# Kernel tuning notes

Hardware: AMD Instinct MI355X
Metric: run time of the kernel (lower is better)

## Reference

```python
import jax, jax.numpy as jnp
import numpy as np

N_NODES = 50000
N_EDGES = 800000
IN_F, HID, OUT = 128, 128, 64


def setup_inputs() -> dict:
    key = jax.random.key(0)
    ks = jax.random.split(key, 12)
    sc = 0.05
    return {
        "features": jax.random.normal(ks[0], (N_NODES, IN_F), jnp.float32),
        "src": jax.random.randint(ks[1], (N_EDGES,), 0, N_NODES, jnp.int32),
        "dst": jax.random.randint(ks[2], (N_EDGES,), 0, N_NODES, jnp.int32),
        "Wself0": jax.random.normal(ks[3], (IN_F, HID), jnp.float32) * sc,
        "Wneigh0": jax.random.normal(ks[4], (IN_F, HID), jnp.float32) * sc,
        "b0": jnp.zeros((HID,), jnp.float32),
        "Wself1": jax.random.normal(ks[5], (HID, HID), jnp.float32) * sc,
        "Wneigh1": jax.random.normal(ks[6], (HID, HID), jnp.float32) * sc,
        "b1": jnp.zeros((HID,), jnp.float32),
        "Wself2": jax.random.normal(ks[7], (HID, OUT), jnp.float32) * sc,
        "Wneigh2": jax.random.normal(ks[8], (HID, OUT), jnp.float32) * sc,
        "b2": jnp.zeros((OUT,), jnp.float32),
    }


def _sage_conv(h, src, dst, Ws, Wn, b, act):
    # mean aggregator: mean over in-neighbors (src -> dst), zero for isolated nodes
    msg = h[src]                                            # [E, d] gather
    agg = jax.ops.segment_sum(msg, dst, num_segments=N_NODES)
    deg = jax.ops.segment_sum(jnp.ones((msg.shape[0],), h.dtype), dst,
                              num_segments=N_NODES)
    mean = agg / jnp.maximum(deg, 1.0)[:, None]             # [N, d]
    out = h @ Ws + mean @ Wn + b                            # fc_self + fc_neigh + bias
    return jax.nn.relu(out) if act else out


def reference(features, src, dst, Wself0, Wneigh0, b0, Wself1, Wneigh1, b1,
              Wself2, Wneigh2, b2):
    h = _sage_conv(features, src, dst, Wself0, Wneigh0, b0, True)
    h = _sage_conv(h, src, dst, Wself1, Wneigh1, b1, True)
    h = _sage_conv(h, src, dst, Wself2, Wneigh2, b2, False)
    return h
```

## Files before the change

### kernel.cpp

```cpp
#include <hip/hip_runtime.h>
#include <hip/hip_fp16.h>

#define N_NODES_C 50000
#define N_EDGES_C 800000
#define K_FEAT 128
#define HM_STRIDE 256
#define NB_C 196

typedef unsigned int uint_t;
typedef _Float16 half8 __attribute__((ext_vector_type(8)));
typedef _Float16 half4 __attribute__((ext_vector_type(4)));
typedef float f32x4 __attribute__((ext_vector_type(4)));


__global__ __launch_bounds__(256) void p1hist_conv_kernel(
    const int* __restrict__ dst, uint_t* __restrict__ histG, int E,
    const float* __restrict__ feat, _Float16* __restrict__ hm0,
    const float* __restrict__ Ws0, const float* __restrict__ Wn0,
    const float* __restrict__ Ws1, const float* __restrict__ Wn1,
    const float* __restrict__ Ws2, const float* __restrict__ Wn2,
    _Float16* __restrict__ WT0, _Float16* __restrict__ WT1, _Float16* __restrict__ WT2) {
    const int t = threadIdx.x, b = blockIdx.x;
    if (b < NB_C) {
        __shared__ uint_t hist[256];
        hist[t] = 0;
        __syncthreads();
        const int base = b * 4096;
#pragma unroll
        for (int j = 0; j < 16; ++j) {
            int idx = base + t + j * 256;
            if (idx < E) atomicAdd(&hist[((uint_t)dst[idx]) >> 8], 1u);
        }
        __syncthreads();
        histG[b * 256 + t] = hist[t];
    } else {
        const int i = (b - NB_C) * 256 + t;
        const int n4 = N_NODES_C * K_FEAT / 4;
        if (i < n4) {
            float4 v = reinterpret_cast<const float4*>(feat)[i];
            int n = i >> 5, c4 = i & 31;
            half4 o;
            o.x = (_Float16)v.x; o.y = (_Float16)v.y; o.z = (_Float16)v.z; o.w = (_Float16)v.w;
            *reinterpret_cast<half4*>(hm0 + (size_t)n * HM_STRIDE + c4 * 4) = o;
        } else {
            int idx = i - n4;
            if (idx >= 81920) return;
            const float* Ws;
            const float* Wn;
            _Float16* WT;
            int ncol;
            if (idx < 32768) { Ws = Ws0; Wn = Wn0; WT = WT0; ncol = 128; }
            else if (idx < 65536) { idx -= 32768; Ws = Ws1; Wn = Wn1; WT = WT1; ncol = 128; }
            else { idx -= 65536; Ws = Ws2; Wn = Wn2; WT = WT2; ncol = 64; }
            int k = idx & 255, c = idx >> 8;
            float v = (k < 128) ? Ws[(size_t)k * ncol + c] : Wn[(size_t)(k - 128) * ncol + c];
            WT[(size_t)c * 256 + k] = (_Float16)v;
        }
    }
}

__global__ __launch_bounds__(256) void p1scan_kernel(uint_t* __restrict__ histG,
                                                     uint_t* __restrict__ cbase) {
    const int t = threadIdx.x;
    uint_t run = 0;
    for (int bb = 0; bb < NB_C; bb += 28) {
        uint_t vals[28];
#pragma unroll
        for (int j = 0; j < 28; ++j) vals[j] = histG[(size_t)(bb + j) * 256 + t];
#pragma unroll
        for (int j = 0; j < 28; ++j) {
            uint_t x = vals[j];
            vals[j] = run;
            run += x;
        }
#pragma unroll
        for (int j = 0; j < 28; ++j) histG[(size_t)(bb + j) * 256 + t] = vals[j];
    }
    const int lane = t & 63, wid = t >> 6;
    uint_t x = run;
#pragma unroll
    for (int off = 1; off < 64; off <<= 1) {
        uint_t y = __shfl_up(x, off, 64);
        if (lane >= off) x += y;
    }
    __shared__ uint_t wsum[4];
    if (lane == 63) wsum[wid] = x;
    __syncthreads();
    uint_t wpre = 0;
#pragma unroll
    for (int w = 0; w < 4; ++w)
        if (w < wid) wpre += wsum[w];
    uint_t incl = wpre + x;
    cbase[t] = incl - run;
    if (t == 255) cbase[256] = incl;
}

__global__ __launch_bounds__(256) void p1scatter_kernel(const int* __restrict__ src,
                                                        const int* __restrict__ dst,
                                                        const uint_t* __restrict__ histG,
                                                        const uint_t* __restrict__ cbase,
                                                        uint_t* __restrict__ tmp, int E) {
    __shared__ uint_t cur[256];
    const int t = threadIdx.x, b = blockIdx.x;
    cur[t] = histG[b * 256 + t] + cbase[t];
    __syncthreads();
    const int base = b * 4096;
#pragma unroll
    for (int j = 0; j < 16; ++j) {
        int idx = base + t + j * 256;
        if (idx < E) {
            uint_t d = (uint_t)dst[idx];
            uint_t s = (uint_t)src[idx];
            uint_t slot = atomicAdd(&cur[d >> 8], 1u);
            tmp[slot] = ((d & 255u) << 16) | s;
        }
    }
}

__global__ __launch_bounds__(256) void p2_kernel(const uint_t* __restrict__ tmp,
                                                 const uint_t* __restrict__ cbase,
                                                 int* __restrict__ offs, int* __restrict__ ssrc) {
    __shared__ uint_t hist[256];
    __shared__ uint_t cur[256];
    __shared__ uint_t wsum[4];
    const int t = threadIdx.x, c = blockIdx.x;
    const uint_t cb = cbase[c], ce = cbase[c + 1];
    hist[t] = 0;
    __syncthreads();
    for (uint_t i = cb + t; i < ce; i += 256) atomicAdd(&hist[tmp[i] >> 16], 1u);
    __syncthreads();
    const uint_t v = hist[t];
    const int lane = t & 63, wid = t >> 6;
    uint_t x = v;
#pragma unroll
    for (int off = 1; off < 64; off <<= 1) {
        uint_t y = __shfl_up(x, off, 64);
        if (lane >= off) x += y;
    }
    if (lane == 63) wsum[wid] = x;
    __syncthreads();
    uint_t wpre = 0;
#pragma unroll
    for (int w = 0; w < 4; ++w)
        if (w < wid) wpre += wsum[w];
    const uint_t excl = wpre + x - v;
    const int node = c * 256 + t;
    if (node < N_NODES_C) offs[node] = (int)(cb + excl);
    if (c == 0 && t == 0) offs[N_NODES_C] = N_EDGES_C;
    cur[t] = excl;
    __syncthreads();
    for (uint_t i = cb + t; i < ce; i += 256) {
        uint_t p = tmp[i];
        uint_t slot = cb + atomicAdd(&cur[p >> 16], 1u);
        ssrc[slot] = (int)(p & 0xFFFFu);
    }
}


__global__ void mean_kernel(_Float16* __restrict__ hm, const int* __restrict__ offs,
                            const int* __restrict__ ssrc) {
    const int node = (int)((blockIdx.x * blockDim.x + threadIdx.x) >> 6);
    const int lane = threadIdx.x & 63;
    if (node >= N_NODES_C) return;
    const int beg = offs[node], end = offs[node + 1];
    const int g = lane >> 4;
    const int cb = (lane & 15) * 8;
    const _Float16* base = hm + cb;

    float accA[8] = {0.f, 0.f, 0.f, 0.f, 0.f, 0.f, 0.f, 0.f};
    float accB[8] = {0.f, 0.f, 0.f, 0.f, 0.f, 0.f, 0.f, 0.f};

    int e = beg;
    for (; e + 16 <= end; e += 16) {
        const int s0 = ssrc[e + g];
        const int s1 = ssrc[e + 4 + g];
        const int s2 = ssrc[e + 8 + g];
        const int s3 = ssrc[e + 12 + g];
        half8 v0 = *reinterpret_cast<const half8*>(base + (size_t)s0 * HM_STRIDE);
        half8 v1 = *reinterpret_cast<const half8*>(base + (size_t)s1 * HM_STRIDE);
        half8 v2 = *reinterpret_cast<const half8*>(base + (size_t)s2 * HM_STRIDE);
        half8 v3 = *reinterpret_cast<const half8*>(base + (size_t)s3 * HM_STRIDE);
#pragma unroll
        for (int j = 0; j < 8; ++j) accA[j] += (float)v0[j];
#pragma unroll
        for (int j = 0; j < 8; ++j) accB[j] += (float)v1[j];
#pragma unroll
        for (int j = 0; j < 8; ++j) accA[j] += (float)v2[j];
#pragma unroll
        for (int j = 0; j < 8; ++j) accB[j] += (float)v3[j];
    }
    for (; e + 8 <= end; e += 8) {
        const int s0 = ssrc[e + g];
        const int s1 = ssrc[e + 4 + g];
        half8 v0 = *reinterpret_cast<const half8*>(base + (size_t)s0 * HM_STRIDE);
        half8 v1 = *reinterpret_cast<const half8*>(base + (size_t)s1 * HM_STRIDE);
#pragma unroll
        for (int j = 0; j < 8; ++j) accA[j] += (float)v0[j];
#pragma unroll
        for (int j = 0; j < 8; ++j) accB[j] += (float)v1[j];
    }
    for (; e + 4 <= end; e += 4) {
        const int s0 = ssrc[e + g];
        half8 v0 = *reinterpret_cast<const half8*>(base + (size_t)s0 * HM_STRIDE);
#pragma unroll
        for (int j = 0; j < 8; ++j) accA[j] += (float)v0[j];
    }
    if (e < end) {
        const bool valid = (e + g) < end;
        const int s0 = valid ? ssrc[e + g] : ssrc[beg];
        half8 v0 = *reinterpret_cast<const half8*>(base + (size_t)s0 * HM_STRIDE);
        if (valid) {
#pragma unroll
            for (int j = 0; j < 8; ++j) accB[j] += (float)v0[j];
        }
    }

    const float inv = (end > beg) ? 1.0f / (float)(end - beg) : 0.f;
    half8 o;
#pragma unroll
    for (int j = 0; j < 8; ++j) {
        float x = accA[j] + accB[j];
        x += __shfl_xor(x, 16, 64);
        x += __shfl_xor(x, 32, 64);
        o[j] = (_Float16)(x * inv);
    }
    if (lane < 16)
        *reinterpret_cast<half8*>(hm + (size_t)node * HM_STRIDE + 128 + cb) = o;
}


template <int NCOL, bool ACT, bool OUT_FP32>
__global__ __launch_bounds__(256) void sage_mfma(
    const _Float16* __restrict__ hm,
    const _Float16* __restrict__ WT,
    const float* __restrict__ bias,
    float* __restrict__ outf,
    _Float16* __restrict__ outh,
    int nNodes) {
    constexpr int CF = NCOL / 16;
    constexpr int RPB = 128;

    __shared__ _Float16 bl[NCOL][256];

    const int t = threadIdx.x;
#pragma unroll
    for (int it = 0; it < NCOL * 32 / 256; ++it) {
        int f = t + it * 256;
        int row = f >> 5, c8 = f & 31;
        half8 v = *reinterpret_cast<const half8*>(WT + (size_t)row * 256 + c8 * 8);
        int col = (c8 * 8) ^ ((row & 7) << 3);
        *reinterpret_cast<half8*>(&bl[row][col]) = v;
    }
    __syncthreads();

    const int wid = t >> 6;
    const int lane = t & 63;
    const int r0 = blockIdx.x * RPB + wid * 32;
    const int koff = (lane >> 4) * 8;

    half8 a[2][8];
#pragma unroll
    for (int fr = 0; fr < 2; ++fr) {
        int row = r0 + fr * 16 + (lane & 15);
        if (row >= nNodes) row = nNodes - 1;
        const _Float16* ap = hm + (size_t)row * HM_STRIDE + koff;
#pragma unroll
        for (int ks = 0; ks < 8; ++ks)
            a[fr][ks] = *reinterpret_cast<const half8*>(ap + ks * 32);
    }

    f32x4 acc[2][CF];
#pragma unroll
    for (int fr = 0; fr < 2; ++fr)
#pragma unroll
        for (int c = 0; c < CF; ++c) acc[fr][c] = {0.f, 0.f, 0.f, 0.f};

#pragma unroll
    for (int c = 0; c < CF; ++c) {
        const int brow = c * 16 + (lane & 15);
        const int bswz = (brow & 7) << 3;
#pragma unroll
        for (int ks = 0; ks < 8; ++ks) {
            half8 b = *reinterpret_cast<const half8*>(&bl[brow][(ks * 32 + koff) ^ bswz]);
            acc[0][c] = __builtin_amdgcn_mfma_f32_16x16x32_f16(a[0][ks], b, acc[0][c], 0, 0, 0);
            acc[1][c] = __builtin_amdgcn_mfma_f32_16x16x32_f16(a[1][ks], b, acc[1][c], 0, 0, 0);
        }
    }

    const int ocol = lane & 15;
    const int orow_off = (lane >> 4) << 2;
#pragma unroll
    for (int fr = 0; fr < 2; ++fr) {
        const int rbase = r0 + fr * 16 + orow_off;
#pragma unroll
        for (int c = 0; c < CF; ++c) {
            const int col = c * 16 + ocol;
            const float bv = bias[col];
#pragma unroll
            for (int reg = 0; reg < 4; ++reg) {
                const int row = rbase + reg;
                if (row < nNodes) {
                    float v = acc[fr][c][reg] + bv;
                    if (ACT) v = fmaxf(v, 0.f);
                    if (OUT_FP32) outf[(size_t)row * NCOL + col] = v;
                    else outh[(size_t)row * HM_STRIDE + col] = (_Float16)v;
                }
            }
        }
    }
}


extern "C" void kernel_launch(void* const* d_in, const int* in_sizes, int n_in,
                              void* d_out, int out_size, void* d_ws, size_t ws_size,
                              hipStream_t stream) {
    const float* feat = (const float*)d_in[0];
    const int* src = (const int*)d_in[1];
    const int* dst = (const int*)d_in[2];
    const float* Ws0 = (const float*)d_in[3];
    const float* Wn0 = (const float*)d_in[4];
    const float* b0 = (const float*)d_in[5];
    const float* Ws1 = (const float*)d_in[6];
    const float* Wn1 = (const float*)d_in[7];
    const float* b1 = (const float*)d_in[8];
    const float* Ws2 = (const float*)d_in[9];
    const float* Wn2 = (const float*)d_in[10];
    const float* b2 = (const float*)d_in[11];
    float* out = (float*)d_out;

    auto align_up = [](size_t x) { return (x + 255) & ~(size_t)255; };
    char* w = (char*)d_ws;
    uint_t* histG = (uint_t*)w; w += align_up((size_t)NB_C * 256 * 4);
    uint_t* cbase = (uint_t*)w; w += align_up(257 * 4);
    uint_t* tmp = (uint_t*)w;   w += align_up((size_t)N_EDGES_C * 4);
    int* offs = (int*)w;        w += align_up((size_t)(N_NODES_C + 1) * 4);
    int* ssrc = (int*)w;        w += align_up((size_t)N_EDGES_C * 4);
    _Float16* hm0 = (_Float16*)w; w += align_up((size_t)N_NODES_C * HM_STRIDE * 2);
    _Float16* hm1 = (_Float16*)w; w += align_up((size_t)N_NODES_C * HM_STRIDE * 2);
    _Float16* WT0 = (_Float16*)w; w += align_up((size_t)128 * 256 * 2);
    _Float16* WT1 = (_Float16*)w; w += align_up((size_t)128 * 256 * 2);
    _Float16* WT2 = (_Float16*)w; w += align_up((size_t)64 * 256 * 2);
    _Float16* hm2 = hm0;

    const int convBlocks = (N_NODES_C * K_FEAT / 4 + 81920 + 255) / 256;
    p1hist_conv_kernel<<<NB_C + convBlocks, 256, 0, stream>>>(
        dst, histG, N_EDGES_C, feat, hm0, Ws0, Wn0, Ws1, Wn1, Ws2, Wn2, WT0, WT1, WT2);
    p1scan_kernel<<<1, 256, 0, stream>>>(histG, cbase);
    p1scatter_kernel<<<NB_C, 256, 0, stream>>>(src, dst, histG, cbase, tmp, N_EDGES_C);
    p2_kernel<<<NB_C, 256, 0, stream>>>(tmp, cbase, offs, ssrc);

    const int meanBlocks = (N_NODES_C * 64 + 255) / 256;
    const int gemmBlocks = (N_NODES_C + 127) / 128;

    mean_kernel<<<meanBlocks, 256, 0, stream>>>(hm0, offs, ssrc);
    sage_mfma<128, true, false><<<gemmBlocks, 256, 0, stream>>>(
        hm0, WT0, b0, nullptr, hm1, N_NODES_C);

    mean_kernel<<<meanBlocks, 256, 0, stream>>>(hm1, offs, ssrc);
    sage_mfma<128, true, false><<<gemmBlocks, 256, 0, stream>>>(
        hm1, WT1, b1, nullptr, hm2, N_NODES_C);

    mean_kernel<<<meanBlocks, 256, 0, stream>>>(hm2, offs, ssrc);
    sage_mfma<64, false, true><<<gemmBlocks, 256, 0, stream>>>(
        hm2, WT2, b2, out, nullptr, N_NODES_C);
}
```

Baseline: 167.6 us.

## Quantize node features to int8 with per-row scales for neighbor gather

Adds a per-node int8 copy of the features with one fp32 scale per row. It is produced in the conversion kernel and in each GEMM epilogue, and the mean aggregation now gathers these 8-byte int8 vectors plus a scale instead of 16-byte fp16 vectors. The aim is to halve the bytes moved by the random neighbor gather, which dominates the mean kernels. The cost is extra quantization stores and shuffles in the epilogues, an extra scale load per edge, and a loss of accuracy from 8-bit features that may exceed tolerance.

New measurement: 154.9 us. 7.6% less time.

```diff
diff --git a/kernel.cpp b/kernel.cpp
--- a/kernel.cpp
+++ b/kernel.cpp
@@ -8,6 +8,8 @@
 #define NB_C 196
 
 typedef unsigned int uint_t;
+typedef signed char schar;
+typedef schar schar8 __attribute__((ext_vector_type(8)));
 typedef _Float16 half8 __attribute__((ext_vector_type(8)));
 typedef _Float16 half4 __attribute__((ext_vector_type(4)));
 typedef float f32x4 __attribute__((ext_vector_type(4)));
@@ -16,6 +18,7 @@
 __global__ __launch_bounds__(256) void p1hist_conv_kernel(
     const int* __restrict__ dst, uint_t* __restrict__ histG, int E,
     const float* __restrict__ feat, _Float16* __restrict__ hm0,
+    schar* __restrict__ q0, float* __restrict__ sc0,
     const float* __restrict__ Ws0, const float* __restrict__ Wn0,
     const float* __restrict__ Ws1, const float* __restrict__ Wn1,
     const float* __restrict__ Ws2, const float* __restrict__ Wn2,
@@ -42,6 +45,19 @@
             half4 o;
             o.x = (_Float16)v.x; o.y = (_Float16)v.y; o.z = (_Float16)v.z; o.w = (_Float16)v.w;
             *reinterpret_cast<half4*>(hm0 + (size_t)n * HM_STRIDE + c4 * 4) = o;
+            float m = fmaxf(fmaxf(fabsf(v.x), fabsf(v.y)), fmaxf(fabsf(v.z), fabsf(v.w)));
+            m = fmaxf(m, __shfl_xor(m, 1, 64));
+            m = fmaxf(m, __shfl_xor(m, 2, 64));
+            m = fmaxf(m, __shfl_xor(m, 4, 64));
+            m = fmaxf(m, __shfl_xor(m, 8, 64));
+            m = fmaxf(m, __shfl_xor(m, 16, 64));
+            const float inv = (m > 0.f) ? 127.0f / m : 0.f;
+            uint_t w = ((uint_t)(unsigned char)(schar)rintf(v.x * inv)) |
+                       ((uint_t)(unsigned char)(schar)rintf(v.y * inv) << 8) |
+                       ((uint_t)(unsigned char)(schar)rintf(v.z * inv) << 16) |
+                       ((uint_t)(unsigned char)(schar)rintf(v.w * inv) << 24);
+            *reinterpret_cast<uint_t*>(q0 + (size_t)n * 128 + c4 * 4) = w;
+            if ((t & 31) == 0) sc0[n] = m * (1.0f / 127.0f);
         } else {
             int idx = i - n4;
             if (idx >= 81920) return;
@@ -157,7 +173,8 @@
 }
 
 
-__global__ void mean_kernel(_Float16* __restrict__ hm, const int* __restrict__ offs,
+__global__ void mean_kernel(const schar* __restrict__ q, const float* __restrict__ qsc,
+                            _Float16* __restrict__ hm, const int* __restrict__ offs,
                             const int* __restrict__ ssrc) {
     const int node = (int)((blockIdx.x * blockDim.x + threadIdx.x) >> 6);
     const int lane = threadIdx.x & 63;
@@ -165,7 +182,7 @@
     const int beg = offs[node], end = offs[node + 1];
     const int g = lane >> 4;
     const int cb = (lane & 15) * 8;
-    const _Float16* base = hm + cb;
+    const schar* base = q + cb;
 
     float accA[8] = {0.f, 0.f, 0.f, 0.f, 0.f, 0.f, 0.f, 0.f};
     float accB[8] = {0.f, 0.f, 0.f, 0.f, 0.f, 0.f, 0.f, 0.f};
@@ -176,43 +193,45 @@
         const int s1 = ssrc[e + 4 + g];
         const int s2 = ssrc[e + 8 + g];
         const int s3 = ssrc[e + 12 + g];
-        half8 v0 = *reinterpret_cast<const half8*>(base + (size_t)s0 * HM_STRIDE);
-        half8 v1 = *reinterpret_cast<const half8*>(base + (size_t)s1 * HM_STRIDE);
-        half8 v2 = *reinterpret_cast<const half8*>(base + (size_t)s2 * HM_STRIDE);
-        half8 v3 = *reinterpret_cast<const half8*>(base + (size_t)s3 * HM_STRIDE);
-#pragma unroll
-        for (int j = 0; j < 8; ++j) accA[j] += (float)v0[j];
-#pragma unroll
-        for (int j = 0; j < 8; ++j) accB[j] += (float)v1[j];
-#pragma unroll
-        for (int j = 0; j < 8; ++j) accA[j] += (float)v2[j];
-#pragma unroll
-        for (int j = 0; j < 8; ++j) accB[j] += (float)v3[j];
+        const float c0 = qsc[s0], c1 = qsc[s1], c2 = qsc[s2], c3 = qsc[s3];
+        schar8 v0 = *reinterpret_cast<const schar8*>(base + (size_t)s0 * 128);
+        schar8 v1 = *reinterpret_cast<const schar8*>(base + (size_t)s1 * 128);
+        schar8 v2 = *reinterpret_cast<const schar8*>(base + (size_t)s2 * 128);
+        schar8 v3 = *reinterpret_cast<const schar8*>(base + (size_t)s3 * 128);
+#pragma unroll
+        for (int j = 0; j < 8; ++j) accA[j] += c0 * (float)v0[j];
+#pragma unroll
+        for (int j = 0; j < 8; ++j) accB[j] += c1 * (float)v1[j];
+#pragma unroll
+        for (int j = 0; j < 8; ++j) accA[j] += c2 * (float)v2[j];
+#pragma unroll
+        for (int j = 0; j < 8; ++j) accB[j] += c3 * (float)v3[j];
     }
     for (; e + 8 <= end; e += 8) {
         const int s0 = ssrc[e + g];
         const int s1 = ssrc[e + 4 + g];
-        half8 v0 = *reinterpret_cast<const half8*>(base + (size_t)s0 * HM_STRIDE);
-        half8 v1 = *reinterpret_cast<const half8*>(base + (size_t)s1 * HM_STRIDE);
-#pragma unroll
-        for (int j = 0; j < 8; ++j) accA[j] += (float)v0[j];
-#pragma unroll
-        for (int j = 0; j < 8; ++j) accB[j] += (float)v1[j];
+        const float c0 = qsc[s0], c1 = qsc[s1];
+        schar8 v0 = *reinterpret_cast<const schar8*>(base + (size_t)s0 * 128);
+        schar8 v1 = *reinterpret_cast<const schar8*>(base + (size_t)s1 * 128);
+#pragma unroll
+        for (int j = 0; j < 8; ++j) accA[j] += c0 * (float)v0[j];
+#pragma unroll
+        for (int j = 0; j < 8; ++j) accB[j] += c1 * (float)v1[j];
     }
     for (; e + 4 <= end; e += 4) {
         const int s0 = ssrc[e + g];
-        half8 v0 = *reinterpret_cast<const half8*>(base + (size_t)s0 * HM_STRIDE);
-#pragma unroll
-        for (int j = 0; j < 8; ++j) accA[j] += (float)v0[j];
+        const float c0 = qsc[s0];
+        schar8 v0 = *reinterpret_cast<const schar8*>(base + (size_t)s0 * 128);
+#pragma unroll
+        for (int j = 0; j < 8; ++j) accA[j] += c0 * (float)v0[j];
     }
     if (e < end) {
         const bool valid = (e + g) < end;
         const int s0 = valid ? ssrc[e + g] : ssrc[beg];
-        half8 v0 = *reinterpret_cast<const half8*>(base + (size_t)s0 * HM_STRIDE);
-        if (valid) {
-#pragma unroll
-            for (int j = 0; j < 8; ++j) accB[j] += (float)v0[j];
-        }
+        const float c0 = valid ? qsc[s0] : 0.f;
+        schar8 v0 = *reinterpret_cast<const schar8*>(base + (size_t)s0 * 128);
+#pragma unroll
+        for (int j = 0; j < 8; ++j) accB[j] += c0 * (float)v0[j];
     }
 
     const float inv = (end > beg) ? 1.0f / (float)(end - beg) : 0.f;
@@ -236,6 +255,8 @@
     const float* __restrict__ bias,
     float* __restrict__ outf,
     _Float16* __restrict__ outh,
+    schar* __restrict__ qout,
+    float* __restrict__ scout,
     int nNodes) {
     constexpr int CF = NCOL / 16;
     constexpr int RPB = 128;
@@ -289,21 +310,44 @@
 
     const int ocol = lane & 15;
     const int orow_off = (lane >> 4) << 2;
+    float bv[CF];
+#pragma unroll
+    for (int c = 0; c < CF; ++c) bv[c] = bias[c * 16 + ocol];
+
 #pragma unroll
     for (int fr = 0; fr < 2; ++fr) {
-        const int rbase = r0 + fr * 16 + orow_off;
-#pragma unroll
-        for (int c = 0; c < CF; ++c) {
-            const int col = c * 16 + ocol;
-            const float bv = bias[col];
-#pragma unroll
-            for (int reg = 0; reg < 4; ++reg) {
-                const int row = rbase + reg;
+#pragma unroll
+        for (int reg = 0; reg < 4; ++reg) {
+            const int row = r0 + fr * 16 + orow_off + reg;
+            float vals[CF];
+            float m = 0.f;
+#pragma unroll
+            for (int c = 0; c < CF; ++c) {
+                float v = acc[fr][c][reg] + bv[c];
+                if (ACT) v = fmaxf(v, 0.f);
+                vals[c] = v;
+                m = fmaxf(m, fabsf(v));
+            }
+            if (OUT_FP32) {
                 if (row < nNodes) {
-                    float v = acc[fr][c][reg] + bv;
-                    if (ACT) v = fmaxf(v, 0.f);
-                    if (OUT_FP32) outf[(size_t)row * NCOL + col] = v;
-                    else outh[(size_t)row * HM_STRIDE + col] = (_Float16)v;
+#pragma unroll
+                    for (int c = 0; c < CF; ++c)
+                        outf[(size_t)row * NCOL + c * 16 + ocol] = vals[c];
+                }
+            } else {
+                m = fmaxf(m, __shfl_xor(m, 1, 64));
+                m = fmaxf(m, __shfl_xor(m, 2, 64));
+                m = fmaxf(m, __shfl_xor(m, 4, 64));
+                m = fmaxf(m, __shfl_xor(m, 8, 64));
+                const float qinv = (m > 0.f) ? 127.0f / m : 0.f;
+                if (row < nNodes) {
+#pragma unroll
+                    for (int c = 0; c < CF; ++c) {
+                        const int col = c * 16 + ocol;
+                        outh[(size_t)row * HM_STRIDE + col] = (_Float16)vals[c];
+                        qout[(size_t)row * 128 + col] = (schar)rintf(vals[c] * qinv);
+                    }
+                    if (ocol == 0) scout[row] = m * (1.0f / 127.0f);
                 }
             }
         }
@@ -337,14 +381,21 @@
     int* ssrc = (int*)w;        w += align_up((size_t)N_EDGES_C * 4);
     _Float16* hm0 = (_Float16*)w; w += align_up((size_t)N_NODES_C * HM_STRIDE * 2);
     _Float16* hm1 = (_Float16*)w; w += align_up((size_t)N_NODES_C * HM_STRIDE * 2);
+    schar* q0 = (schar*)w;      w += align_up((size_t)N_NODES_C * 128);
+    schar* q1 = (schar*)w;      w += align_up((size_t)N_NODES_C * 128);
+    float* sc0 = (float*)w;     w += align_up((size_t)N_NODES_C * 4);
+    float* sc1 = (float*)w;     w += align_up((size_t)N_NODES_C * 4);
     _Float16* WT0 = (_Float16*)w; w += align_up((size_t)128 * 256 * 2);
     _Float16* WT1 = (_Float16*)w; w += align_up((size_t)128 * 256 * 2);
     _Float16* WT2 = (_Float16*)w; w += align_up((size_t)64 * 256 * 2);
     _Float16* hm2 = hm0;
+    schar* q2 = q0;
+    float* sc2 = sc0;
 
     const int convBlocks = (N_NODES_C * K_FEAT / 4 + 81920 + 255) / 256;
     p1hist_conv_kernel<<<NB_C + convBlocks, 256, 0, stream>>>(
-        dst, histG, N_EDGES_C, feat, hm0, Ws0, Wn0, Ws1, Wn1, Ws2, Wn2, WT0, WT1, WT2);
+        dst, histG, N_EDGES_C, feat, hm0, q0, sc0,
+        Ws0, Wn0, Ws1, Wn1, Ws2, Wn2, WT0, WT1, WT2);
     p1scan_kernel<<<1, 256, 0, stream>>>(histG, cbase);
     p1scatter_kernel<<<NB_C, 256, 0, stream>>>(src, dst, histG, cbase, tmp, N_EDGES_C);
     p2_kernel<<<NB_C, 256, 0, stream>>>(tmp, cbase, offs, ssrc);
@@ -352,15 +403,15 @@
     const int meanBlocks = (N_NODES_C * 64 + 255) / 256;
     const int gemmBlocks = (N_NODES_C + 127) / 128;
 
-    mean_kernel<<<meanBlocks, 256, 0, stream>>>(hm0, offs, ssrc);
+    mean_kernel<<<meanBlocks, 256, 0, stream>>>(q0, sc0, hm0, offs, ssrc);
     sage_mfma<128, true, false><<<gemmBlocks, 256, 0, stream>>>(
-        hm0, WT0, b0, nullptr, hm1, N_NODES_C);
-
-    mean_kernel<<<meanBlocks, 256, 0, stream>>>(hm1, offs, ssrc);
+        hm0, WT0, b0, nullptr, hm1, q1, sc1, N_NODES_C);
+
+    mean_kernel<<<meanBlocks, 256, 0, stream>>>(q1, sc1, hm1, offs, ssrc);
     sage_mfma<128, true, false><<<gemmBlocks, 256, 0, stream>>>(
-        hm1, WT1, b1, nullptr, hm2, N_NODES_C);
-
-    mean_kernel<<<meanBlocks, 256, 0, stream>>>(hm2, offs, ssrc);
+        hm1, WT1, b1, nullptr, hm2, q2, sc2, N_NODES_C);
+
+    mean_kernel<<<meanBlocks, 256, 0, stream>>>(q2, sc2, hm2, offs, ssrc);
     sage_mfma<64, false, true><<<gemmBlocks, 256, 0, stream>>>(
-        hm2, WT2, b2, out, nullptr, N_NODES_C);
-}
+        hm2, WT2, b2, out, nullptr, nullptr, nullptr, N_NODES_C);
+}
```
